# Kernel tuning notes

Measured on AMD Instinct MI355X. Metric: run time of the kernel, lower is better.

## Reference

```python
import jax, jax.numpy as jnp
import numpy as np

D_MODEL = 1024
N_HEADS = 16
D_K = D_MODEL // N_HEADS
THETA = 10000.0
B, S = 2, 2048


def _rope(x):
    # x: [B, H, S, Dh], interleaved-pair RoPE with positions arange(S)
    Dh = x.shape[-1]
    inv_freq = 1.0 / (THETA ** (jnp.arange(0, Dh, 2, dtype=jnp.float32) / Dh))  # [Dh/2]
    pos = jnp.arange(x.shape[-2], dtype=jnp.float32)
    ang = pos[:, None] * inv_freq[None, :]                      # [S, Dh/2]
    cos = jnp.repeat(jnp.cos(ang), 2, axis=-1).astype(x.dtype)  # [S, Dh]
    sin = jnp.repeat(jnp.sin(ang), 2, axis=-1).astype(x.dtype)
    # rotate pairs: (x_2k, x_2k+1) -> (-x_2k+1, x_2k)
    xp = x.reshape(*x.shape[:-1], Dh // 2, 2)
    rot = jnp.stack((-xp[..., 1], xp[..., 0]), axis=-1).reshape(x.shape)
    return x * cos + rot * sin


def setup_inputs() -> dict:
    key = jax.random.key(0)
    ks = jax.random.split(key, 5)
    std = (2.0 / (D_MODEL + D_MODEL)) ** 0.5
    return {
        "x": jax.random.normal(ks[0], (B, S, D_MODEL), dtype=jnp.float32),
        "wq": jax.random.normal(ks[1], (D_MODEL, D_MODEL), dtype=jnp.float32) * std,
        "wk": jax.random.normal(ks[2], (D_MODEL, D_MODEL), dtype=jnp.float32) * std,
        "wv": jax.random.normal(ks[3], (D_MODEL, D_MODEL), dtype=jnp.float32) * std,
        "wo": jax.random.normal(ks[4], (D_MODEL, D_MODEL), dtype=jnp.float32) * std,
    }


def reference(x, wq, wk, wv, wo):
    b, s, _ = x.shape
    def split_heads(t):
        return t.reshape(b, s, N_HEADS, D_K).transpose(0, 2, 1, 3)  # [B,H,S,Dk]
    # Linear: y = x @ W.T  (weights stored [out, in])
    q = split_heads(jnp.einsum('bsd,od->bso', x, wq))
    k = split_heads(jnp.einsum('bsd,od->bso', x, wk))
    v = split_heads(jnp.einsum('bsd,od->bso', x, wv))
    q = _rope(q)
    k = _rope(k)
    scores = jnp.einsum('bhqd,bhkd->bhqk', q, k) / jnp.sqrt(jnp.asarray(D_K, x.dtype))
    causal = jnp.tril(jnp.ones((s, s), dtype=bool))
    scores = jnp.where(causal[None, None], scores, -jnp.inf)
    attn = jax.nn.softmax(scores, axis=-1)
    out = jnp.einsum('bhqk,bhkd->bhqd', attn, v)
    out = out.transpose(0, 2, 1, 3).reshape(b, s, D_MODEL)
    return jnp.einsum('bsd,od->bso', out, wo)
```

## Files before the change

kernel.cpp:

```cpp
#include <hip/hip_runtime.h>


typedef unsigned short u16;
typedef __attribute__((ext_vector_type(8))) short short8;
typedef __attribute__((ext_vector_type(4))) float float4v;

typedef const __attribute__((address_space(1))) void GV;
typedef __attribute__((address_space(3))) void LV;

#define VSTR 72
#define QSCL 0.18033688011112042f

__device__ __forceinline__ u16 f2b(float f) {
    union { float f; unsigned int i; } t; t.f = f;
    unsigned int r = t.i + 0x7fffu + ((t.i >> 16) & 1u);
    return (u16)(r >> 16);
}

__global__ __launch_bounds__(256) void cvt_all(
    const float4* __restrict__ x,  const float4* __restrict__ wq,
    const float4* __restrict__ wk, const float4* __restrict__ wv,
    const float4* __restrict__ wo,
    u16* __restrict__ xb, u16* __restrict__ wcat, u16* __restrict__ wob)
{
    const int i = blockIdx.x * 256 + threadIdx.x;
    const float4* s; u16* d; int off;
    if (i < 524288) { s = x; d = xb; off = i; }
    else {
        const int widx = i - 524288;
        const int w = widx >> 17, o = widx & 131071;
        switch (w) {
            case 0:  s = wq; d = wcat;              break;
            case 1:  s = wk; d = wcat + (1 << 20);  break;
            case 2:  s = wv; d = wcat + (2 << 20);  break;
            default: s = wo; d = wob;               break;
        }
        off = o;
    }
    float4 a = s[2 * off], b = s[2 * off + 1];
    u16 t[8] = {f2b(a.x), f2b(a.y), f2b(a.z), f2b(a.w),
                f2b(b.x), f2b(b.y), f2b(b.z), f2b(b.w)};
    reinterpret_cast<int4*>(d)[off] = *reinterpret_cast<int4*>(t);
}

__global__ __launch_bounds__(256) void rope_tab(float2* __restrict__ tab) {
    const int i = blockIdx.x * 256 + threadIdx.x;
    const int pos = i >> 5, fi = i & 31;
    const float freq = exp2f((float)fi * -0.4152410118609203f);
    float sn, cs; sincosf((float)pos * freq, &sn, &cs);
    tab[i] = make_float2(cs, sn);
}

template<int NT, int ROPE, int NBLK>
__global__ __launch_bounds__(256) void gemm_tile(
    const u16* __restrict__ X, const u16* __restrict__ Wb,
    u16* __restrict__ Yq, u16* __restrict__ Yk, u16* __restrict__ Yv,
    float* __restrict__ Yf, const float2* __restrict__ tab)
{
    __shared__ u16 As[128 * 64];
    __shared__ u16 Bs[NT * 32 * 64];

    const int tid  = threadIdx.x;
    const int wave = tid >> 6;
    const int lane = tid & 63;
    const int quad = lane >> 4;
    const int l16  = lane & 15;
    const int wm = (wave >> 1) * 64, wn = (wave & 1) * (NT * 16);
    const int g = blockIdx.x;
    const int rr = g >> 3;
    const int m0 = ((g & 7) * 4 + rr / NBLK) * 128;
    const int n0 = (rr % NBLK) * (NT * 32);
    const int lrow = lane >> 3;
    const int cg8  = (lane & 7) ^ lrow;

    float4v acc[4][NT];
#pragma unroll
    for (int mt = 0; mt < 4; mt++)
#pragma unroll
        for (int nt = 0; nt < NT; nt++) acc[mt][nt] = (float4v){0.f, 0.f, 0.f, 0.f};

    for (int kb = 0; kb < 1024; kb += 64) {
        __syncthreads();
#pragma unroll
        for (int t = 0; t < 4; t++) {
            const int I = wave * 4 + t;
            const u16* gp = X + (size_t)(m0 + I * 8 + lrow) * 1024 + kb + cg8 * 8;
            __builtin_amdgcn_global_load_lds((GV*)gp, (LV*)&As[I * 512], 16, 0, 0);
        }
#pragma unroll
        for (int t = 0; t < NT; t++) {
            const int I = wave * NT + t;
            const u16* gp = Wb + (size_t)(n0 + I * 8 + lrow) * 1024 + kb + cg8 * 8;
            __builtin_amdgcn_global_load_lds((GV*)gp, (LV*)&Bs[I * 512], 16, 0, 0);
        }
        __syncthreads();
#pragma unroll
        for (int ks = 0; ks < 2; ks++) {
            const int su = ((ks * 4 + quad) ^ (l16 & 7)) * 8;
            short8 af[4], bf[NT];
#pragma unroll
            for (int t = 0; t < 4; t++)
                af[t] = *reinterpret_cast<const short8*>(&As[(wm + t * 16 + l16) * 64 + su]);
#pragma unroll
            for (int t = 0; t < NT; t++)
                bf[t] = *reinterpret_cast<const short8*>(&Bs[(wn + t * 16 + l16) * 64 + su]);
#pragma unroll
            for (int mt = 0; mt < 4; mt++)
#pragma unroll
                for (int nt = 0; nt < NT; nt++)
                    acc[mt][nt] = __builtin_amdgcn_mfma_f32_16x16x32_bf16(af[mt], bf[nt], acc[mt][nt], 0, 0, 0);
        }
    }

    if (ROPE) {
#pragma unroll
        for (int nt = 0; nt < NT; nt++) {
            const int cg = n0 + wn + nt * 16 + l16;
            const int buf = cg >> 10;
            const int c = cg & 1023;
            u16* dst = (buf == 0) ? Yq : ((buf == 1) ? Yk : Yv);
            const bool rp = (buf < 2);
            const float scl = (buf == 0) ? QSCL : 1.0f;
            const int fi = (cg & 63) >> 1;
#pragma unroll
            for (int mt = 0; mt < 4; mt++)
#pragma unroll
                for (int r = 0; r < 4; r++) {
                    const int row = m0 + wm + mt * 16 + quad * 4 + r;
                    float v = acc[mt][nt][r];
                    if (rp) {
                        const float2 t = tab[((row & 2047) << 5) + fi];
                        const float partner = __shfl_xor(v, 1);
                        v = (l16 & 1) ? fmaf(v, t.x,  partner * t.y)
                                      : fmaf(v, t.x, -partner * t.y);
                    }
                    dst[(size_t)row * 1024 + c] = f2b(v * scl);
                }
        }
    } else {
#pragma unroll
        for (int nt = 0; nt < NT; nt++) {
            const int col = n0 + wn + nt * 16 + l16;
#pragma unroll
            for (int mt = 0; mt < 4; mt++)
#pragma unroll
                for (int r = 0; r < 4; r++) {
                    const int row = m0 + wm + mt * 16 + quad * 4 + r;
                    Yf[(size_t)row * 1024 + col] = acc[mt][nt][r];
                }
        }
    }
}

__global__ __launch_bounds__(256, 2) void attn_kernel(
    const u16* Q, const u16* __restrict__ K,
    const u16* __restrict__ V, u16* O)
{
    __shared__ __align__(16) u16 Vt[2][64 * VSTR];

    const int tid  = threadIdx.x;
    const int wave = tid >> 6;
    const int lane = tid & 63;
    const int quad = lane >> 4;
    const int l16  = lane & 15;
    const int g = blockIdx.x;
    const int xcd = g & 7, slot = g >> 3;
    const int G = (slot >> 4) * 8 + xcd;
    const int qtA = slot & 15;
    const int qtB = 31 - qtA;
    const int b = G & 1, h = G >> 1;
    const size_t base = ((size_t)b * 2048) * 1024 + (size_t)h * 64;

    short8 qfA[2], qfB[2];
    {
        const size_t ra = base + (size_t)(qtA * 64 + wave * 16 + l16) * 1024;
        qfA[0] = *reinterpret_cast<const short8*>(Q + ra + quad * 8);
        qfA[1] = *reinterpret_cast<const short8*>(Q + ra + 32 + quad * 8);
        const size_t rb = base + (size_t)(qtB * 64 + wave * 16 + l16) * 1024;
        qfB[0] = *reinterpret_cast<const short8*>(Q + rb + quad * 8);
        qfB[1] = *reinterpret_cast<const short8*>(Q + rb + 32 + quad * 8);
    }

    float4v oA[4], oB[4];
#pragma unroll
    for (int i = 0; i < 4; i++) { oA[i] = (float4v){0.f,0.f,0.f,0.f}; oB[i] = (float4v){0.f,0.f,0.f,0.f}; }
    float sA = 0.f, sB = 0.f;

    const int srow = tid >> 2;
    const int cb   = (tid & 3) << 4;
    const int sxw  = srow ^ cb;

    const u16* Vp = V + base + (size_t)srow * 1024 + cb;
    const u16* kbase = K + base + (size_t)l16 * 1024 + quad * 8;
    int4 vr0 = *reinterpret_cast<const int4*>(Vp);
    int4 vr1 = *reinterpret_cast<const int4*>(Vp + 8);
    short8 kn[4][2], kc[4][2], vf[4][2];
#pragma unroll
    for (int nt = 0; nt < 4; nt++)
#pragma unroll
        for (int ks = 0; ks < 2; ks++)
            kn[nt][ks] = *reinterpret_cast<const short8*>(kbase + (size_t)(nt * 16) * 1024 + ks * 32);

    {
        const u16* a = reinterpret_cast<const u16*>(&vr0);
        const u16* c = reinterpret_cast<const u16*>(&vr1);
#pragma unroll
        for (int e = 0; e < 8; e++) Vt[0][(cb + e) * VSTR + sxw] = a[e];
#pragma unroll
        for (int e = 0; e < 8; e++) Vt[0][(cb + 8 + e) * VSTR + sxw] = c[e];
    }
    vr0 = *reinterpret_cast<const int4*>(Vp + 65536);
    vr1 = *reinterpret_cast<const int4*>(Vp + 65536 + 8);

    const int qloc = wave * 16 + l16;

    auto qk = [&](const short8 (&qf)[2], float4v (&sacc)[4]) {
#pragma unroll
        for (int nt = 0; nt < 4; nt++) {
            sacc[nt] = (float4v){0.f, 0.f, 0.f, 0.f};
#pragma unroll
            for (int ks = 0; ks < 2; ks++)
                sacc[nt] = __builtin_amdgcn_mfma_f32_16x16x32_bf16(kc[nt][ks], qf[ks], sacc[nt], 0, 0, 0);
        }
    };
    auto smx = [&](const float4v (&sacc)[4], float &sr, short8 (&pa)[2], bool diag) {
        unsigned int w[4][2];
#pragma unroll
        for (int nt = 0; nt < 4; nt++) {
            float p[4];
#pragma unroll
            for (int r = 0; r < 4; r++) {
                float sv = sacc[nt][r];
                if (diag && (nt * 16 + quad * 4 + r > qloc)) sv = -1e30f;
                p[r] = exp2f(sv);
                sr += p[r];
            }
            asm("v_cvt_pk_bf16_f32 %0, %1, %2" : "=v"(w[nt][0]) : "v"(p[0]), "v"(p[1]));
            asm("v_cvt_pk_bf16_f32 %0, %1, %2" : "=v"(w[nt][1]) : "v"(p[2]), "v"(p[3]));
        }
        union { unsigned int u[4]; short8 s8; } t;
        t.u[0] = w[0][0]; t.u[1] = w[0][1]; t.u[2] = w[1][0]; t.u[3] = w[1][1];
        pa[0] = t.s8;
        t.u[0] = w[2][0]; t.u[1] = w[2][1]; t.u[2] = w[3][0]; t.u[3] = w[3][1];
        pa[1] = t.s8;
    };
    auto pv = [&](const short8 (&pa)[2], float4v (&oc)[4]) {
#pragma unroll
        for (int ks = 0; ks < 2; ks++)
#pragma unroll
            for (int dt = 0; dt < 4; dt++)
                oc[dt] = __builtin_amdgcn_mfma_f32_16x16x32_bf16(pa[ks], vf[dt][ks], oc[dt], 0, 0, 0);
    };

    for (int j = 0; j <= qtB; j++) {
        __syncthreads();
        if (j < qtB) {
            u16* D = Vt[(j + 1) & 1];
            const u16* a = reinterpret_cast<const u16*>(&vr0);
            const u16* c = reinterpret_cast<const u16*>(&vr1);
#pragma unroll
            for (int e = 0; e < 8; e++) D[(cb + e) * VSTR + sxw] = a[e];
#pragma unroll
            for (int e = 0; e < 8; e++) D[(cb + 8 + e) * VSTR + sxw] = c[e];
        }
#pragma unroll
        for (int nt = 0; nt < 4; nt++)
#pragma unroll
            for (int ks = 0; ks < 2; ks++) kc[nt][ks] = kn[nt][ks];
        if (j < qtB) {
            if (j + 2 <= qtB) {
                vr0 = *reinterpret_cast<const int4*>(Vp + (size_t)(j + 2) * 65536);
                vr1 = *reinterpret_cast<const int4*>(Vp + (size_t)(j + 2) * 65536 + 8);
            }
            const u16* kb2 = kbase + (size_t)(j + 1) * 65536;
#pragma unroll
            for (int nt = 0; nt < 4; nt++)
#pragma unroll
                for (int ks = 0; ks < 2; ks++)
                    kn[nt][ks] = *reinterpret_cast<const short8*>(kb2 + (size_t)(nt * 16) * 1024 + ks * 32);
        }
        {
            const u16* B = Vt[j & 1];
#pragma unroll
            for (int dt = 0; dt < 4; dt++) {
                const int rb = (dt * 16 + l16) * VSTR;
#pragma unroll
                for (int ks = 0; ks < 2; ks++) {
                    const int k1 = (ks * 32 + quad * 4) ^ (dt << 4);
                    const int k2 = (ks * 32 + 16 + quad * 4) ^ (dt << 4);
                    union { struct { uint2 lo, hi; } p; short8 s8; } u;
                    u.p.lo = *reinterpret_cast<const uint2*>(&B[rb + k1]);
                    u.p.hi = *reinterpret_cast<const uint2*>(&B[rb + k2]);
                    vf[dt][ks] = u.s8;
                }
            }
        }

        if (j <= qtA) {
            float4v xA[4], xB[4];
            qk(qfA, xA);
            qk(qfB, xB);
            short8 paA[2], paB[2];
            smx(xA, sA, paA, j == qtA);
            smx(xB, sB, paB, false);
            pv(paA, oA);
            pv(paB, oB);
        } else {
            float4v xB[4];
            qk(qfB, xB);
            short8 paB[2];
            smx(xB, sB, paB, j == qtB);
            pv(paB, oB);
        }
    }

    float tA = sA, tB = sB;
    tA += __shfl_xor(tA, 16); tA += __shfl_xor(tA, 32);
    tB += __shfl_xor(tB, 16); tB += __shfl_xor(tB, 32);
#pragma unroll
    for (int r = 0; r < 4; r++) {
        const int rl = quad * 4 + r;
        const float invA = 1.0f / __shfl(tA, rl);
        const float invB = 1.0f / __shfl(tB, rl);
        const size_t rowA = base + (size_t)(qtA * 64 + wave * 16 + rl) * 1024;
        const size_t rowB = base + (size_t)(qtB * 64 + wave * 16 + rl) * 1024;
#pragma unroll
        for (int dt = 0; dt < 4; dt++) {
            O[rowA + dt * 16 + l16] = f2b(oA[dt][r] * invA);
            O[rowB + dt * 16 + l16] = f2b(oB[dt][r] * invB);
        }
    }
}

extern "C" void kernel_launch(void* const* d_in, const int* in_sizes, int n_in,
                              void* d_out, int out_size, void* d_ws, size_t ws_size,
                              hipStream_t stream) {
    (void)in_sizes; (void)n_in; (void)out_size; (void)ws_size;
    const float* x  = (const float*)d_in[0];
    const float* wq = (const float*)d_in[1];
    const float* wk = (const float*)d_in[2];
    const float* wv = (const float*)d_in[3];
    const float* wo = (const float*)d_in[4];

    const size_t MN = (size_t)4096 * 1024;

    u16* xb   = (u16*)d_out;
    u16* wcat = xb + MN;
    float2* tab = (float2*)(wcat + (size_t)3072 * 1024);
    u16* qbuf = (u16*)d_ws;
    u16* kbuf = qbuf + MN;
    u16* vbuf = kbuf + MN;
    u16* wob  = vbuf + MN;

    cvt_all<<<4096, 256, 0, stream>>>((const float4*)x, (const float4*)wq,
                                      (const float4*)wk, (const float4*)wv,
                                      (const float4*)wo, xb, wcat, wob);
    rope_tab<<<256, 256, 0, stream>>>(tab);
    gemm_tile<4, 1, 24><<<768, 256, 0, stream>>>(xb, wcat, qbuf, kbuf, vbuf, nullptr, tab);
    attn_kernel<<<512, 256, 0, stream>>>(qbuf, kbuf, vbuf, qbuf);
    gemm_tile<2, 0, 16><<<512, 256, 0, stream>>>(qbuf, wob, nullptr, nullptr, nullptr, (float*)d_out, nullptr);
}
```

Before: 229.5 us.

## Add dedicated double-buffered 256x192 QKV GEMM kernel with 512 threads

```diff
diff --git a/kernel.cpp b/kernel.cpp
--- a/kernel.cpp
+++ b/kernel.cpp
@@ -51,11 +51,104 @@
     tab[i] = make_float2(cs, sn);
 }
 
-template<int NT, int ROPE, int NBLK>
+__global__ __launch_bounds__(512) void gemm_qkv(
+    const u16* __restrict__ X, const u16* __restrict__ Wb,
+    u16* __restrict__ Yq, u16* __restrict__ Yk, u16* __restrict__ Yv,
+    const float2* __restrict__ tab)
+{
+    __shared__ u16 As[2][256 * 64];
+    __shared__ u16 Bs[2][192 * 64];
+
+    const int tid  = threadIdx.x;
+    const int wave = tid >> 6;
+    const int lane = tid & 63;
+    const int quad = lane >> 4;
+    const int l16  = lane & 15;
+    const int wm = (wave >> 2) * 128;
+    const int wn = (wave & 3) * 48;
+    const int g = blockIdx.x;
+    const int rr = g >> 3;
+    const int m0 = ((g & 7) * 2 + (rr >> 4)) * 256;
+    const int n0 = (rr & 15) * 192;
+    const int lrow = lane >> 3;
+    const int cg8  = (lane & 7) ^ lrow;
+
+    float4v acc[8][3];
+#pragma unroll
+    for (int mt = 0; mt < 8; mt++)
+#pragma unroll
+        for (int nt = 0; nt < 3; nt++) acc[mt][nt] = (float4v){0.f, 0.f, 0.f, 0.f};
+
+    auto stage = [&](int bsel, int kb) {
+#pragma unroll
+        for (int t = 0; t < 4; t++) {
+            const int I = wave * 4 + t;
+            const u16* gp = X + (size_t)(m0 + I * 8 + lrow) * 1024 + kb + cg8 * 8;
+            __builtin_amdgcn_global_load_lds((GV*)gp, (LV*)&As[bsel][I * 512], 16, 0, 0);
+        }
+#pragma unroll
+        for (int t = 0; t < 3; t++) {
+            const int I = wave * 3 + t;
+            const u16* gp = Wb + (size_t)(n0 + I * 8 + lrow) * 1024 + kb + cg8 * 8;
+            __builtin_amdgcn_global_load_lds((GV*)gp, (LV*)&Bs[bsel][I * 512], 16, 0, 0);
+        }
+    };
+
+    stage(0, 0);
+    __syncthreads();
+
+    for (int kbi = 0; kbi < 16; kbi++) {
+        const int cur = kbi & 1;
+        if (kbi < 15) stage(cur ^ 1, (kbi + 1) * 64);
+#pragma unroll
+        for (int ks = 0; ks < 2; ks++) {
+            const int su = ((ks * 4 + quad) ^ (l16 & 7)) * 8;
+            short8 af[8], bf[3];
+#pragma unroll
+            for (int t = 0; t < 8; t++)
+                af[t] = *reinterpret_cast<const short8*>(&As[cur][(wm + t * 16 + l16) * 64 + su]);
+#pragma unroll
+            for (int t = 0; t < 3; t++)
+                bf[t] = *reinterpret_cast<const short8*>(&Bs[cur][(wn + t * 16 + l16) * 64 + su]);
+#pragma unroll
+            for (int mt = 0; mt < 8; mt++)
+#pragma unroll
+                for (int nt = 0; nt < 3; nt++)
+                    acc[mt][nt] = __builtin_amdgcn_mfma_f32_16x16x32_bf16(af[mt], bf[nt], acc[mt][nt], 0, 0, 0);
+        }
+        __syncthreads();
+    }
+
+#pragma unroll
+    for (int nt = 0; nt < 3; nt++) {
+        const int cg = n0 + wn + nt * 16 + l16;
+        const int buf = cg >> 10;
+        const int c = cg & 1023;
+        u16* dst = (buf == 0) ? Yq : ((buf == 1) ? Yk : Yv);
+        const bool rp = (buf < 2);
+        const float scl = (buf == 0) ? QSCL : 1.0f;
+        const int fi = (cg & 63) >> 1;
+#pragma unroll
+        for (int mt = 0; mt < 8; mt++)
+#pragma unroll
+            for (int r = 0; r < 4; r++) {
+                const int row = m0 + wm + mt * 16 + quad * 4 + r;
+                float v = acc[mt][nt][r];
+                if (rp) {
+                    const float2 t = tab[((row & 2047) << 5) + fi];
+                    const float partner = __shfl_xor(v, 1);
+                    v = (l16 & 1) ? fmaf(v, t.x,  partner * t.y)
+                                  : fmaf(v, t.x, -partner * t.y);
+                }
+                dst[(size_t)row * 1024 + c] = f2b(v * scl);
+            }
+    }
+}
+
+template<int NT, int NBLK>
 __global__ __launch_bounds__(256) void gemm_tile(
     const u16* __restrict__ X, const u16* __restrict__ Wb,
-    u16* __restrict__ Yq, u16* __restrict__ Yk, u16* __restrict__ Yv,
-    float* __restrict__ Yf, const float2* __restrict__ tab)
+    float* __restrict__ Yf)
 {
     __shared__ u16 As[128 * 64];
     __shared__ u16 Bs[NT * 32 * 64];
@@ -112,43 +205,16 @@
         }
     }
 
-    if (ROPE) {
-#pragma unroll
-        for (int nt = 0; nt < NT; nt++) {
-            const int cg = n0 + wn + nt * 16 + l16;
-            const int buf = cg >> 10;
-            const int c = cg & 1023;
-            u16* dst = (buf == 0) ? Yq : ((buf == 1) ? Yk : Yv);
-            const bool rp = (buf < 2);
-            const float scl = (buf == 0) ? QSCL : 1.0f;
-            const int fi = (cg & 63) >> 1;
-#pragma unroll
-            for (int mt = 0; mt < 4; mt++)
-#pragma unroll
-                for (int r = 0; r < 4; r++) {
-                    const int row = m0 + wm + mt * 16 + quad * 4 + r;
-                    float v = acc[mt][nt][r];
-                    if (rp) {
-                        const float2 t = tab[((row & 2047) << 5) + fi];
-                        const float partner = __shfl_xor(v, 1);
-                        v = (l16 & 1) ? fmaf(v, t.x,  partner * t.y)
-                                      : fmaf(v, t.x, -partner * t.y);
-                    }
-                    dst[(size_t)row * 1024 + c] = f2b(v * scl);
-                }
-        }
-    } else {
-#pragma unroll
-        for (int nt = 0; nt < NT; nt++) {
-            const int col = n0 + wn + nt * 16 + l16;
-#pragma unroll
-            for (int mt = 0; mt < 4; mt++)
-#pragma unroll
-                for (int r = 0; r < 4; r++) {
-                    const int row = m0 + wm + mt * 16 + quad * 4 + r;
-                    Yf[(size_t)row * 1024 + col] = acc[mt][nt][r];
-                }
-        }
+#pragma unroll
+    for (int nt = 0; nt < NT; nt++) {
+        const int col = n0 + wn + nt * 16 + l16;
+#pragma unroll
+        for (int mt = 0; mt < 4; mt++)
+#pragma unroll
+            for (int r = 0; r < 4; r++) {
+                const int row = m0 + wm + mt * 16 + quad * 4 + r;
+                Yf[(size_t)row * 1024 + col] = acc[mt][nt][r];
+            }
     }
 }
 
@@ -356,7 +422,7 @@
                                       (const float4*)wk, (const float4*)wv,
                                       (const float4*)wo, xb, wcat, wob);
     rope_tab<<<256, 256, 0, stream>>>(tab);
-    gemm_tile<4, 1, 24><<<768, 256, 0, stream>>>(xb, wcat, qbuf, kbuf, vbuf, nullptr, tab);
+    gemm_qkv<<<256, 512, 0, stream>>>(xb, wcat, qbuf, kbuf, vbuf, tab);
     attn_kernel<<<512, 256, 0, stream>>>(qbuf, kbuf, vbuf, qbuf);
-    gemm_tile<2, 0, 16><<<512, 256, 0, stream>>>(qbuf, wob, nullptr, nullptr, nullptr, (float*)d_out, nullptr);
-}
+    gemm_tile<2, 16><<<512, 256, 0, stream>>>(qbuf, wob, (float*)d_out);
+}
```

Result: faster. 217.4 us (-5.3%).
